# Performance work log

Hardware: AMD Instinct MI355X
Metric: run time of the kernel (lower is better)

## Reference

```python
import jax, jax.numpy as jnp
import numpy as np


def setup_inputs() -> dict:
    key = jax.random.key(0)
    k1, k2 = jax.random.split(key)
    B, N, M, D = 1, 4096, 4096, 32
    i1 = jax.random.normal(k1, (B, N, D), dtype=jnp.float32)
    i2 = jax.random.normal(k2, (B, M, D), dtype=jnp.float32)
    return {"i1": i1, "i2": i2}


def reference(i1, i2):
    # Faithful to tf: exp(-sum((i1[..., :, None, :] - i2[..., None, :, :])**2, -1) / 2)
    d = i1[..., :, None, :] - i2[..., None, :, :]   # [B, N, M, D]
    sq = jnp.sum(d * d, axis=-1)                    # [B, N, M]
    return jnp.exp(-sq / 2.0)
```

## Files before the change

### kernel.cpp

```cpp
#include <hip/hip_runtime.h>


#define DD 32
#define BT 128
#define KP 40

typedef __attribute__((ext_vector_type(8))) short bfrag8;
typedef __attribute__((ext_vector_type(4))) float f32x4;

__device__ __forceinline__ unsigned short f2bf_rn(float f) {
    unsigned u = __builtin_bit_cast(unsigned, f);
    u += 0x7FFFu + ((u >> 16) & 1u);
    return (unsigned short)(u >> 16);
}
__device__ __forceinline__ float bf2f(unsigned short h) {
    unsigned u = ((unsigned)h) << 16;
    return __builtin_bit_cast(float, u);
}

__global__ __launch_bounds__(256) void rbf_mfma_kernel(
    const float* __restrict__ A,
    const float* __restrict__ B,
    float* __restrict__ out,
    int M)
{
    __shared__ unsigned short sAh[BT][KP];
    __shared__ unsigned short sAl[BT][KP];
    __shared__ unsigned short sBh[BT][KP];
    __shared__ unsigned short sBl[BT][KP];

    const int tid  = threadIdx.x;
    const int brow = blockIdx.y * BT;
    const int bcol = blockIdx.x * BT;

    const float4* gA = reinterpret_cast<const float4*>(A + (size_t)brow * DD);
    const float4* gB = reinterpret_cast<const float4*>(B + (size_t)bcol * DD);

    #pragma unroll
    for (int k = 0; k < 4; ++k) {
        const int i   = tid + k * 256;
        const int row = i >> 3;
        const int d0  = (i & 7) << 2;
        float4 va = gA[i], vb = gB[i];
        ushort4 ha, la, hb, lb;
        ha.x = f2bf_rn(va.x); la.x = f2bf_rn(va.x - bf2f(ha.x));
        ha.y = f2bf_rn(va.y); la.y = f2bf_rn(va.y - bf2f(ha.y));
        ha.z = f2bf_rn(va.z); la.z = f2bf_rn(va.z - bf2f(ha.z));
        ha.w = f2bf_rn(va.w); la.w = f2bf_rn(va.w - bf2f(ha.w));
        hb.x = f2bf_rn(vb.x); lb.x = f2bf_rn(vb.x - bf2f(hb.x));
        hb.y = f2bf_rn(vb.y); lb.y = f2bf_rn(vb.y - bf2f(hb.y));
        hb.z = f2bf_rn(vb.z); lb.z = f2bf_rn(vb.z - bf2f(hb.z));
        hb.w = f2bf_rn(vb.w); lb.w = f2bf_rn(vb.w - bf2f(hb.w));
        *reinterpret_cast<ushort4*>(&sAh[row][d0]) = ha;
        *reinterpret_cast<ushort4*>(&sAl[row][d0]) = la;
        *reinterpret_cast<ushort4*>(&sBh[row][d0]) = hb;
        *reinterpret_cast<ushort4*>(&sBl[row][d0]) = lb;
    }

    {
        const int r = tid & 127;
        const float4* src = (tid < 128)
            ? reinterpret_cast<const float4*>(A + (size_t)(brow + r) * DD)
            : reinterpret_cast<const float4*>(B + (size_t)(bcol + r) * DD);
        float s = 0.f;
        #pragma unroll
        for (int q = 0; q < 8; ++q) {
            float4 v = src[q];
            s += v.x * v.x + v.y * v.y + v.z * v.z + v.w * v.w;
        }
        unsigned short* dst = (tid < 128) ? &sAh[r][32] : &sBh[r][32];
        *reinterpret_cast<float*>(dst) = 0.5f * s;
    }
    __syncthreads();

    const int lane = tid & 63, wid = tid >> 6;
    const int r0 = wid * 32;
    const int lr = lane & 15;
    const int lg = lane >> 4;
    const int k0 = lg * 8;

    const bfrag8 ah0 = *reinterpret_cast<const bfrag8*>(&sAh[r0 + lr][k0]);
    const bfrag8 al0 = *reinterpret_cast<const bfrag8*>(&sAl[r0 + lr][k0]);
    const bfrag8 ah1 = *reinterpret_cast<const bfrag8*>(&sAh[r0 + 16 + lr][k0]);
    const bfrag8 al1 = *reinterpret_cast<const bfrag8*>(&sAl[r0 + 16 + lr][k0]);

    float hna0[4], hna1[4];
    #pragma unroll
    for (int q = 0; q < 4; ++q) {
        hna0[q] = *reinterpret_cast<const float*>(&sAh[r0 + lg * 4 + q][32]);
        hna1[q] = *reinterpret_cast<const float*>(&sAh[r0 + 16 + lg * 4 + q][32]);
    }

    const size_t orow0 = (size_t)(brow + r0 + lg * 4) * M + bcol;

    #pragma unroll
    for (int c = 0; c < 8; ++c) {
        const int c0 = c * 16;
        const bfrag8 bh = *reinterpret_cast<const bfrag8*>(&sBh[c0 + lr][k0]);
        const bfrag8 bl = *reinterpret_cast<const bfrag8*>(&sBl[c0 + lr][k0]);
        const float hnb = *reinterpret_cast<const float*>(&sBh[c0 + lr][32]);

        f32x4 acc0 = {0.f, 0.f, 0.f, 0.f}, acc1 = {0.f, 0.f, 0.f, 0.f};
        acc0 = __builtin_amdgcn_mfma_f32_16x16x32_bf16(al0, bh, acc0, 0, 0, 0);
        acc1 = __builtin_amdgcn_mfma_f32_16x16x32_bf16(al1, bh, acc1, 0, 0, 0);
        acc0 = __builtin_amdgcn_mfma_f32_16x16x32_bf16(ah0, bl, acc0, 0, 0, 0);
        acc1 = __builtin_amdgcn_mfma_f32_16x16x32_bf16(ah1, bl, acc1, 0, 0, 0);
        acc0 = __builtin_amdgcn_mfma_f32_16x16x32_bf16(ah0, bh, acc0, 0, 0, 0);
        acc1 = __builtin_amdgcn_mfma_f32_16x16x32_bf16(ah1, bh, acc1, 0, 0, 0);

        float* p0 = out + orow0 + c0 + lr;
        #pragma unroll
        for (int q = 0; q < 4; ++q) {
            p0[(size_t)q * M]        = __expf(acc0[q] - hna0[q] - hnb);
            p0[(size_t)(q + 16) * M] = __expf(acc1[q] - hna1[q] - hnb);
        }
    }
}

extern "C" void kernel_launch(void* const* d_in, const int* in_sizes, int n_in,
                              void* d_out, int out_size, void* d_ws, size_t ws_size,
                              hipStream_t stream) {
    const float* A = (const float*)d_in[0];
    const float* B = (const float*)d_in[1];
    float* out     = (float*)d_out;
    const int N = in_sizes[0] / DD;
    const int M = in_sizes[1] / DD;
    dim3 grid(M / BT, N / BT);
    rbf_mfma_kernel<<<grid, 256, 0, stream>>>(A, B, out, M);
}
```

Measured before the change: 81.84 us.

## Precompute bf16 hi/lo splits and norms in a prepass kernel, drop LDS staging

```diff
diff --git a/kernel.cpp b/kernel.cpp
--- a/kernel.cpp
+++ b/kernel.cpp
@@ -3,7 +3,6 @@
 
 #define DD 32
 #define BT 128
-#define KP 40
 
 typedef __attribute__((ext_vector_type(8))) short bfrag8;
 typedef __attribute__((ext_vector_type(4))) float f32x4;
@@ -18,101 +17,85 @@
     return __builtin_bit_cast(float, u);
 }
 
-__global__ __launch_bounds__(256) void rbf_mfma_kernel(
-    const float* __restrict__ A,
-    const float* __restrict__ B,
-    float* __restrict__ out,
-    int M)
+__global__ __launch_bounds__(64) void rbf_pre_kernel(
+    const float* __restrict__ A, const float* __restrict__ B,
+    unsigned short* __restrict__ ah, unsigned short* __restrict__ al,
+    unsigned short* __restrict__ bh, unsigned short* __restrict__ bl,
+    float* __restrict__ nhA, float* __restrict__ nhB, int N)
 {
-    __shared__ unsigned short sAh[BT][KP];
-    __shared__ unsigned short sAl[BT][KP];
-    __shared__ unsigned short sBh[BT][KP];
-    __shared__ unsigned short sBl[BT][KP];
+    const int r   = blockIdx.x * 64 + threadIdx.x;
+    const bool isB = r >= N;
+    const int row = isB ? r - N : r;
+    const float4* src = reinterpret_cast<const float4*>((isB ? B : A) + (size_t)row * DD);
+    unsigned short* dh = (isB ? bh : ah) + (size_t)row * DD;
+    unsigned short* dl = (isB ? bl : al) + (size_t)row * DD;
+    float s = 0.f;
+    #pragma unroll
+    for (int q = 0; q < 8; ++q) {
+        float4 v = src[q];
+        s += v.x * v.x + v.y * v.y + v.z * v.z + v.w * v.w;
+        ushort4 h, l;
+        h.x = f2bf_rn(v.x); l.x = f2bf_rn(v.x - bf2f(h.x));
+        h.y = f2bf_rn(v.y); l.y = f2bf_rn(v.y - bf2f(h.y));
+        h.z = f2bf_rn(v.z); l.z = f2bf_rn(v.z - bf2f(h.z));
+        h.w = f2bf_rn(v.w); l.w = f2bf_rn(v.w - bf2f(h.w));
+        *reinterpret_cast<ushort4*>(dh + q * 4) = h;
+        *reinterpret_cast<ushort4*>(dl + q * 4) = l;
+    }
+    ((isB ? nhB : nhA))[row] = -0.5f * s;
+}
 
+__global__ __launch_bounds__(256, 4) void rbf_mfma2_kernel(
+    const unsigned short* __restrict__ ah, const unsigned short* __restrict__ al,
+    const unsigned short* __restrict__ bh, const unsigned short* __restrict__ bl,
+    const float* __restrict__ nhA, const float* __restrict__ nhB,
+    float* __restrict__ out, int M)
+{
     const int tid  = threadIdx.x;
     const int brow = blockIdx.y * BT;
     const int bcol = blockIdx.x * BT;
-
-    const float4* gA = reinterpret_cast<const float4*>(A + (size_t)brow * DD);
-    const float4* gB = reinterpret_cast<const float4*>(B + (size_t)bcol * DD);
-
-    #pragma unroll
-    for (int k = 0; k < 4; ++k) {
-        const int i   = tid + k * 256;
-        const int row = i >> 3;
-        const int d0  = (i & 7) << 2;
-        float4 va = gA[i], vb = gB[i];
-        ushort4 ha, la, hb, lb;
-        ha.x = f2bf_rn(va.x); la.x = f2bf_rn(va.x - bf2f(ha.x));
-        ha.y = f2bf_rn(va.y); la.y = f2bf_rn(va.y - bf2f(ha.y));
-        ha.z = f2bf_rn(va.z); la.z = f2bf_rn(va.z - bf2f(ha.z));
-        ha.w = f2bf_rn(va.w); la.w = f2bf_rn(va.w - bf2f(ha.w));
-        hb.x = f2bf_rn(vb.x); lb.x = f2bf_rn(vb.x - bf2f(hb.x));
-        hb.y = f2bf_rn(vb.y); lb.y = f2bf_rn(vb.y - bf2f(hb.y));
-        hb.z = f2bf_rn(vb.z); lb.z = f2bf_rn(vb.z - bf2f(hb.z));
-        hb.w = f2bf_rn(vb.w); lb.w = f2bf_rn(vb.w - bf2f(hb.w));
-        *reinterpret_cast<ushort4*>(&sAh[row][d0]) = ha;
-        *reinterpret_cast<ushort4*>(&sAl[row][d0]) = la;
-        *reinterpret_cast<ushort4*>(&sBh[row][d0]) = hb;
-        *reinterpret_cast<ushort4*>(&sBl[row][d0]) = lb;
-    }
-
-    {
-        const int r = tid & 127;
-        const float4* src = (tid < 128)
-            ? reinterpret_cast<const float4*>(A + (size_t)(brow + r) * DD)
-            : reinterpret_cast<const float4*>(B + (size_t)(bcol + r) * DD);
-        float s = 0.f;
-        #pragma unroll
-        for (int q = 0; q < 8; ++q) {
-            float4 v = src[q];
-            s += v.x * v.x + v.y * v.y + v.z * v.z + v.w * v.w;
-        }
-        unsigned short* dst = (tid < 128) ? &sAh[r][32] : &sBh[r][32];
-        *reinterpret_cast<float*>(dst) = 0.5f * s;
-    }
-    __syncthreads();
-
     const int lane = tid & 63, wid = tid >> 6;
     const int r0 = wid * 32;
     const int lr = lane & 15;
     const int lg = lane >> 4;
     const int k0 = lg * 8;
 
-    const bfrag8 ah0 = *reinterpret_cast<const bfrag8*>(&sAh[r0 + lr][k0]);
-    const bfrag8 al0 = *reinterpret_cast<const bfrag8*>(&sAl[r0 + lr][k0]);
-    const bfrag8 ah1 = *reinterpret_cast<const bfrag8*>(&sAh[r0 + 16 + lr][k0]);
-    const bfrag8 al1 = *reinterpret_cast<const bfrag8*>(&sAl[r0 + 16 + lr][k0]);
+    const size_t arow = (size_t)(brow + r0 + lr) * DD + k0;
+    const bfrag8 ah0 = *reinterpret_cast<const bfrag8*>(ah + arow);
+    const bfrag8 al0 = *reinterpret_cast<const bfrag8*>(al + arow);
+    const bfrag8 ah1 = *reinterpret_cast<const bfrag8*>(ah + arow + (size_t)16 * DD);
+    const bfrag8 al1 = *reinterpret_cast<const bfrag8*>(al + arow + (size_t)16 * DD);
 
-    float hna0[4], hna1[4];
+    float nha0[4], nha1[4];
     #pragma unroll
     for (int q = 0; q < 4; ++q) {
-        hna0[q] = *reinterpret_cast<const float*>(&sAh[r0 + lg * 4 + q][32]);
-        hna1[q] = *reinterpret_cast<const float*>(&sAh[r0 + 16 + lg * 4 + q][32]);
+        nha0[q] = nhA[brow + r0 + lg * 4 + q];
+        nha1[q] = nhA[brow + r0 + 16 + lg * 4 + q];
     }
 
     const size_t orow0 = (size_t)(brow + r0 + lg * 4) * M + bcol;
 
-    #pragma unroll
+    #pragma unroll 2
     for (int c = 0; c < 8; ++c) {
         const int c0 = c * 16;
-        const bfrag8 bh = *reinterpret_cast<const bfrag8*>(&sBh[c0 + lr][k0]);
-        const bfrag8 bl = *reinterpret_cast<const bfrag8*>(&sBl[c0 + lr][k0]);
-        const float hnb = *reinterpret_cast<const float*>(&sBh[c0 + lr][32]);
+        const size_t brow_off = (size_t)(bcol + c0 + lr) * DD + k0;
+        const bfrag8 bhf = *reinterpret_cast<const bfrag8*>(bh + brow_off);
+        const bfrag8 blf = *reinterpret_cast<const bfrag8*>(bl + brow_off);
+        const float nhb = nhB[bcol + c0 + lr];
 
         f32x4 acc0 = {0.f, 0.f, 0.f, 0.f}, acc1 = {0.f, 0.f, 0.f, 0.f};
-        acc0 = __builtin_amdgcn_mfma_f32_16x16x32_bf16(al0, bh, acc0, 0, 0, 0);
-        acc1 = __builtin_amdgcn_mfma_f32_16x16x32_bf16(al1, bh, acc1, 0, 0, 0);
-        acc0 = __builtin_amdgcn_mfma_f32_16x16x32_bf16(ah0, bl, acc0, 0, 0, 0);
-        acc1 = __builtin_amdgcn_mfma_f32_16x16x32_bf16(ah1, bl, acc1, 0, 0, 0);
-        acc0 = __builtin_amdgcn_mfma_f32_16x16x32_bf16(ah0, bh, acc0, 0, 0, 0);
-        acc1 = __builtin_amdgcn_mfma_f32_16x16x32_bf16(ah1, bh, acc1, 0, 0, 0);
+        acc0 = __builtin_amdgcn_mfma_f32_16x16x32_bf16(al0, bhf, acc0, 0, 0, 0);
+        acc1 = __builtin_amdgcn_mfma_f32_16x16x32_bf16(al1, bhf, acc1, 0, 0, 0);
+        acc0 = __builtin_amdgcn_mfma_f32_16x16x32_bf16(ah0, blf, acc0, 0, 0, 0);
+        acc1 = __builtin_amdgcn_mfma_f32_16x16x32_bf16(ah1, blf, acc1, 0, 0, 0);
+        acc0 = __builtin_amdgcn_mfma_f32_16x16x32_bf16(ah0, bhf, acc0, 0, 0, 0);
+        acc1 = __builtin_amdgcn_mfma_f32_16x16x32_bf16(ah1, bhf, acc1, 0, 0, 0);
 
         float* p0 = out + orow0 + c0 + lr;
         #pragma unroll
         for (int q = 0; q < 4; ++q) {
-            p0[(size_t)q * M]        = __expf(acc0[q] - hna0[q] - hnb);
-            p0[(size_t)(q + 16) * M] = __expf(acc1[q] - hna1[q] - hnb);
+            p0[(size_t)q * M]        = __expf(acc0[q] + nha0[q] + nhb);
+            p0[(size_t)(q + 16) * M] = __expf(acc1[q] + nha1[q] + nhb);
         }
     }
 }
@@ -125,6 +108,16 @@
     float* out     = (float*)d_out;
     const int N = in_sizes[0] / DD;
     const int M = in_sizes[1] / DD;
+
+    char* ws = (char*)d_ws;
+    unsigned short* ah = (unsigned short*)(ws);
+    unsigned short* al = (unsigned short*)(ws + 0x40000);
+    unsigned short* bh = (unsigned short*)(ws + 0x80000);
+    unsigned short* bl = (unsigned short*)(ws + 0xC0000);
+    float* nhA = (float*)(ws + 0x100000);
+    float* nhB = (float*)(ws + 0x104000);
+
+    rbf_pre_kernel<<<(N + M) / 64, 64, 0, stream>>>(A, B, ah, al, bh, bl, nhA, nhB, N);
     dim3 grid(M / BT, N / BT);
-    rbf_mfma_kernel<<<grid, 256, 0, stream>>>(A, B, out, M);
+    rbf_mfma2_kernel<<<grid, 256, 0, stream>>>(ah, al, bh, bl, nhA, nhB, out, M);
 }
```

Result: no change. 82.57 us (+0.9%).
